# Kernel tuning notes

Measured on AMD Instinct MI355X. Metric: run time of the kernel, lower is better.

## Reference

```python
import jax, jax.numpy as jnp
import numpy as np

K = 7      # local attention window (kernel_size)
PAD = 3    # padding = (K - 1) // 2 so unfold output matches input spatial size
EPS = 1e-5 # BatchNorm eps


def conv1x1(x, w, b):
    # x: [B,C,H,W], w: [O,C] -> [B,O,H,W]
    return jnp.einsum('bchw,oc->bohw', x, w) + b[None, :, None, None]


def bn(x, g, beta, m, v):
    # inference-mode BatchNorm2d
    s = g / jnp.sqrt(v + EPS)
    return (x - m[None, :, None, None]) * s[None, :, None, None] + beta[None, :, None, None]


def unfold(x):
    # F.unfold(kernel=K, pad=PAD, stride=1) reshaped to [B, C, K*K, H, W]
    b, c, h, w = x.shape
    xp = jnp.pad(x, ((0, 0), (0, 0), (PAD, PAD), (PAD, PAD)))
    return jnp.stack([xp[:, :, i:i + h, j:j + w]
                      for i in range(K) for j in range(K)], axis=2)


def setup_inputs() -> dict:
    key = jax.random.key(0)
    ks = jax.random.split(key, 17)
    B, C, H, W = 2, 256, 96, 96
    KC, VC, OC = 64, 128, 256

    def n(k, shape, s=0.05):
        return jax.random.normal(k, shape, dtype=jnp.float32) * s

    return {
        'x': jax.random.normal(ks[0], (B, C, H, W), dtype=jnp.float32),
        'wq': n(ks[1], (KC, C)), 'bq': n(ks[2], (KC,)),
        'gq': 1.0 + n(ks[3], (KC,)), 'betaq': n(ks[4], (KC,)),
        'mq': n(ks[5], (KC,)),
        'vq': jax.random.uniform(ks[6], (KC,), dtype=jnp.float32, minval=0.5, maxval=1.5),
        'wk': n(ks[7], (KC, C)), 'bk': n(ks[8], (KC,)),
        'gk': 1.0 + n(ks[9], (KC,)), 'betak': n(ks[10], (KC,)),
        'mk': n(ks[11], (KC,)),
        'vk': jax.random.uniform(ks[12], (KC,), dtype=jnp.float32, minval=0.5, maxval=1.5),
        'wv': n(ks[13], (VC, C)), 'bv': n(ks[14], (VC,)),
        'ww': n(ks[15], (OC, VC)), 'bw': n(ks[16], (OC,)),
    }


def reference(x, wq, bq, gq, betaq, mq, vq, wk, bk, gk, betak, mk, vk, wv, bv, ww, bw):
    value = conv1x1(x, wv, bv)                       # [B,VC,H,W]
    uv = unfold(value)                                # [B,VC,K*K,H,W]
    keyf = bn(conv1x1(x, wk, bk), gk, betak, mk, vk)  # [B,KC,H,W]
    uk = unfold(keyf)                                 # [B,KC,K*K,H,W]
    query = bn(conv1x1(x, wq, bq), gq, betaq, mq, vq) # [B,KC,H,W]
    # sim_map = sum over channels of (unfold_key * query), softmax over patch dim
    sim = jnp.einsum('bcphw,bchw->bphw', uk, query)   # [B,K*K,H,W]
    sm = jax.nn.softmax(sim, axis=1)
    context = jnp.einsum('bphw,bcphw->bchw', sm, uv)  # [B,VC,H,W]
    return conv1x1(context, ww, bw)                   # [B,OC,H,W]
```

## Files before the change

kernel.cpp:

```cpp
#include <hip/hip_runtime.h>
#include <hip/hip_bf16.h>
#include <cstddef>


#define HW 9216
#define IMH 96
#define IMW 96

__global__ __launch_bounds__(256) void prep_kernel(
    const float* __restrict__ wq, const float* __restrict__ bq,
    const float* __restrict__ gq, const float* __restrict__ betaq,
    const float* __restrict__ mq, const float* __restrict__ vq,
    const float* __restrict__ wk, const float* __restrict__ bk,
    const float* __restrict__ gk, const float* __restrict__ betak,
    const float* __restrict__ mk, const float* __restrict__ vk,
    const float* __restrict__ wv, const float* __restrict__ bv,
    float* __restrict__ Weff, float* __restrict__ beff) {
  int o = blockIdx.x;
  int c = threadIdx.x;
  float wval, bval;
  if (o < 64) {
    float s = gq[o] * rsqrtf(vq[o] + 1e-5f);
    wval = wq[o * 256 + c] * s;
    bval = (bq[o] - mq[o]) * s + betaq[o];
  } else if (o < 128) {
    int oo = o - 64;
    float s = gk[oo] * rsqrtf(vk[oo] + 1e-5f);
    wval = wk[oo * 256 + c] * s;
    bval = (bk[oo] - mk[oo]) * s + betak[oo];
  } else {
    int oo = o - 128;
    wval = wv[oo * 256 + c];
    bval = bv[oo];
  }
  Weff[o * 256 + c] = wval;
  if (c == 0) beff[o] = bval;
}

template <int KD>
__global__ __launch_bounds__(256) void gemm_tile(
    const float* __restrict__ A, const float* __restrict__ bias,
    const float* __restrict__ X, float* __restrict__ O, long xbstride) {
  int b = blockIdx.z;
  int m0 = blockIdx.y * 64;
  int n0 = blockIdx.x * 64;
  const float* Xb = X + (size_t)b * xbstride;
  float* Ob = O + (size_t)b * 256 * HW;

  __shared__ float As[16][68];
  __shared__ float Bs[16][68];

  int tid = threadIdx.x;
  int tx = tid & 15;
  int ty = tid >> 4;

  float acc[4][4];
#pragma unroll
  for (int i = 0; i < 4; i++)
#pragma unroll
    for (int j = 0; j < 4; j++) acc[i][j] = 0.f;

  for (int kk = 0; kk < KD; kk += 16) {
#pragma unroll
    for (int i = 0; i < 4; i++) {
      int idx = tid + i * 256;
      int m = idx >> 4, k = idx & 15;
      As[k][m] = A[(size_t)(m0 + m) * KD + kk + k];
    }
#pragma unroll
    for (int i = 0; i < 4; i++) {
      int idx = tid + i * 256;
      int k = idx >> 6, n = idx & 63;
      Bs[k][n] = Xb[(size_t)(kk + k) * HW + n0 + n];
    }
    __syncthreads();
#pragma unroll
    for (int k = 0; k < 16; k++) {
      float4 av = *(const float4*)&As[k][ty * 4];
      float4 bv4 = *(const float4*)&Bs[k][tx * 4];
      float a_[4] = {av.x, av.y, av.z, av.w};
      float b_[4] = {bv4.x, bv4.y, bv4.z, bv4.w};
#pragma unroll
      for (int i = 0; i < 4; i++)
#pragma unroll
        for (int j = 0; j < 4; j++) acc[i][j] = fmaf(a_[i], b_[j], acc[i][j]);
    }
    __syncthreads();
  }

#pragma unroll
  for (int i = 0; i < 4; i++) {
    int m = m0 + ty * 4 + i;
    float bs = bias[m];
    float4 r;
    r.x = acc[i][0] + bs;
    r.y = acc[i][1] + bs;
    r.z = acc[i][2] + bs;
    r.w = acc[i][3] + bs;
    *(float4*)&Ob[(size_t)m * HW + n0 + tx * 4] = r;
  }
}

__global__ __launch_bounds__(64) void sim_kernel(
    const float* __restrict__ qkv, float* __restrict__ sm) {
  int b = blockIdx.z;
  int tap = blockIdx.y;
  int pix = blockIdx.x * 64 + threadIdx.x;
  int h = pix / IMW, w = pix % IMW;
  int di = tap / 7 - 3, dj = tap % 7 - 3;
  const float* Qp = qkv + (size_t)b * 256 * HW + pix;
  const float* Kp = Qp + (size_t)64 * HW + di * IMW + dj;

  float a0 = 0.f, a1 = 0.f, a2 = 0.f, a3 = 0.f;
#pragma unroll 8
  for (int c = 0; c < 64; c++) {
    float q = Qp[(size_t)c * HW];
    float k = Kp[(size_t)c * HW];
    if ((c & 3) == 0) a0 = fmaf(q, k, a0);
    else if ((c & 3) == 1) a1 = fmaf(q, k, a1);
    else if ((c & 3) == 2) a2 = fmaf(q, k, a2);
    else a3 = fmaf(q, k, a3);
  }
  float s = (a0 + a1) + (a2 + a3);
  bool valid = ((unsigned)(h + di) < (unsigned)IMH) &&
               ((unsigned)(w + dj) < (unsigned)IMW);
  sm[((size_t)b * 49 + tap) * HW + pix] = valid ? s : 0.f;
}

__global__ __launch_bounds__(64) void softmax_kernel(float* __restrict__ sm) {
  int b = blockIdx.y;
  int pix = blockIdx.x * 64 + threadIdx.x;
  int h = pix / IMW, w = pix % IMW;
  float* S = sm + (size_t)b * 49 * HW + pix;

  float v[49];
#pragma unroll
  for (int p = 0; p < 49; p++) v[p] = S[(size_t)p * HW];

  float mx = v[0];
#pragma unroll
  for (int p = 1; p < 49; p++) mx = fmaxf(mx, v[p]);
  float ssum = 0.f;
#pragma unroll
  for (int p = 0; p < 49; p++) {
    v[p] = __expf(v[p] - mx);
    ssum += v[p];
  }
  float inv = 1.f / ssum;
#pragma unroll
  for (int p = 0; p < 49; p++) {
    const int di = p / 7 - 3, dj = p % 7 - 3;
    bool valid = ((unsigned)(h + di) < (unsigned)IMH) &&
                 ((unsigned)(w + dj) < (unsigned)IMW);
    S[(size_t)p * HW] = valid ? v[p] * inv : 0.f;
  }
}

__global__ __launch_bounds__(64) void ctx_kernel(
    const float* __restrict__ qkv, const float* __restrict__ sm,
    float* __restrict__ ctx) {
  int b = blockIdx.z;
  int c0 = blockIdx.y * 4;
  int pix = blockIdx.x * 64 + threadIdx.x;

  const float* S = sm + (size_t)b * 49 * HW + pix;
  float p[49];
#pragma unroll
  for (int t = 0; t < 49; t++) p[t] = S[(size_t)t * HW];

  const float* V = qkv + ((size_t)b * 256 + 128) * HW + pix;
  float* Cb = ctx + (size_t)b * 256 * HW + pix;

#pragma unroll
  for (int cc = 0; cc < 4; cc++) {
    const float* Vc = V + (size_t)(c0 + cc) * HW;
    float a0 = 0.f, a1 = 0.f, a2 = 0.f, a3 = 0.f;
#pragma unroll
    for (int t = 0; t < 49; t++) {
      const int di = t / 7 - 3, dj = t % 7 - 3;
      float v = Vc[di * IMW + dj];
      if ((t & 3) == 0) a0 = fmaf(p[t], v, a0);
      else if ((t & 3) == 1) a1 = fmaf(p[t], v, a1);
      else if ((t & 3) == 2) a2 = fmaf(p[t], v, a2);
      else a3 = fmaf(p[t], v, a3);
    }
    Cb[(size_t)(c0 + cc) * HW] = (a0 + a1) + (a2 + a3);
  }
}

extern "C" void kernel_launch(void* const* d_in, const int* in_sizes, int n_in,
                              void* d_out, int out_size, void* d_ws, size_t ws_size,
                              hipStream_t stream) {
  const float* x     = (const float*)d_in[0];
  const float* wq    = (const float*)d_in[1];
  const float* bq    = (const float*)d_in[2];
  const float* gq    = (const float*)d_in[3];
  const float* betaq = (const float*)d_in[4];
  const float* mq    = (const float*)d_in[5];
  const float* vq    = (const float*)d_in[6];
  const float* wk    = (const float*)d_in[7];
  const float* bk    = (const float*)d_in[8];
  const float* gk    = (const float*)d_in[9];
  const float* betak = (const float*)d_in[10];
  const float* mk    = (const float*)d_in[11];
  const float* vk    = (const float*)d_in[12];
  const float* wv    = (const float*)d_in[13];
  const float* bv    = (const float*)d_in[14];
  const float* ww    = (const float*)d_in[15];
  const float* bw    = (const float*)d_in[16];

  float* ws = (float*)d_ws;
  float* Weff = ws;
  float* beff = ws + 65536;
  float* qkv  = ws + 65792;
  float* sm   = ws + 65792 + 4718592 + 1024;
  float* ctxb = qkv;

  prep_kernel<<<dim3(256), dim3(256), 0, stream>>>(
      wq, bq, gq, betaq, mq, vq, wk, bk, gk, betak, mk, vk, wv, bv, Weff, beff);

  gemm_tile<256><<<dim3(144, 4, 2), dim3(256), 0, stream>>>(
      Weff, beff, x, qkv, (long)256 * HW);

  sim_kernel<<<dim3(144, 49, 2), dim3(64), 0, stream>>>(qkv, sm);

  softmax_kernel<<<dim3(144, 2), dim3(64), 0, stream>>>(sm);

  ctx_kernel<<<dim3(144, 32, 2), dim3(64), 0, stream>>>(qkv, sm, ctxb);

  gemm_tile<128><<<dim3(144, 4, 2), dim3(256), 0, stream>>>(
      ww, bw, ctxb, (float*)d_out, (long)256 * HW);
}
```

Measured before the change: 204.7 us.

## Replace FP32 SIMT GEMMs with split-bf16 MFMA GEMMs plus transpose-convert passes

Both 1x1-conv GEMMs now run on bf16 MFMA instructions. Each fp32 operand is split into hi and lo bf16 parts, and three products (hi*hi, lo*hi, hi*lo) are accumulated to keep close to fp32 accuracy. New transpose-and-convert kernels write the activations in pixel-major bf16 hi/lo form, and the prep kernel also splits the weights. This adds extra memory passes and kernel launches and triples the MFMA work, in exchange for much higher matrix throughput than the FMA-based tiles.

```diff
diff --git a/kernel.cpp b/kernel.cpp
--- a/kernel.cpp
+++ b/kernel.cpp
@@ -6,6 +6,19 @@
 #define HW 9216
 #define IMH 96
 #define IMW 96
+
+using bf16x8 = __attribute__((ext_vector_type(8))) short;
+using f32x4  = __attribute__((ext_vector_type(4))) float;
+
+__device__ inline unsigned short f2bf(float f) {
+  unsigned u = __builtin_bit_cast(unsigned, f);
+  unsigned r = 0x7fffu + ((u >> 16) & 1u);
+  return (unsigned short)((u + r) >> 16);
+}
+__device__ inline float bf2f(unsigned short h) {
+  unsigned u = (unsigned)h << 16;
+  return __builtin_bit_cast(float, u);
+}
 
 __global__ __launch_bounds__(256) void prep_kernel(
     const float* __restrict__ wq, const float* __restrict__ bq,
@@ -15,7 +28,10 @@
     const float* __restrict__ gk, const float* __restrict__ betak,
     const float* __restrict__ mk, const float* __restrict__ vk,
     const float* __restrict__ wv, const float* __restrict__ bv,
-    float* __restrict__ Weff, float* __restrict__ beff) {
+    const float* __restrict__ ww,
+    unsigned short* __restrict__ WeffHi, unsigned short* __restrict__ WeffLo,
+    float* __restrict__ beff,
+    unsigned short* __restrict__ wwHi, unsigned short* __restrict__ wwLo) {
   int o = blockIdx.x;
   int c = threadIdx.x;
   float wval, bval;
@@ -33,71 +49,124 @@
     wval = wv[oo * 256 + c];
     bval = bv[oo];
   }
-  Weff[o * 256 + c] = wval;
+  unsigned short hi = f2bf(wval);
+  WeffHi[o * 256 + c] = hi;
+  WeffLo[o * 256 + c] = f2bf(wval - bf2f(hi));
   if (c == 0) beff[o] = bval;
+  if (c < 128) {
+    float wv2 = ww[o * 128 + c];
+    unsigned short h2 = f2bf(wv2);
+    wwHi[o * 128 + c] = h2;
+    wwLo[o * 128 + c] = f2bf(wv2 - bf2f(h2));
+  }
+}
+
+template <int C>
+__global__ __launch_bounds__(256) void tcvt_kernel(
+    const float* __restrict__ in,
+    unsigned short* __restrict__ outHi, unsigned short* __restrict__ outLo) {
+  int b = blockIdx.z;
+  int c0 = blockIdx.y * 64;
+  int p0 = blockIdx.x * 64;
+  const float* ib = in + (size_t)b * C * HW;
+  unsigned short* obh = outHi + (size_t)b * HW * C;
+  unsigned short* obl = outLo + (size_t)b * HW * C;
+  __shared__ float t[64][65];
+  int tid = threadIdx.x;
+#pragma unroll
+  for (int i = 0; i < 16; i++) {
+    int idx = tid + i * 256;
+    int c = idx >> 6, p = idx & 63;
+    t[c][p] = ib[(size_t)(c0 + c) * HW + p0 + p];
+  }
+  __syncthreads();
+#pragma unroll
+  for (int i = 0; i < 16; i++) {
+    int idx = tid + i * 256;
+    int p = idx >> 6, c = idx & 63;
+    float v = t[c][p];
+    unsigned short hi = f2bf(v);
+    size_t o = (size_t)(p0 + p) * C + c0 + c;
+    obh[o] = hi;
+    obl[o] = f2bf(v - bf2f(hi));
+  }
 }
 
 template <int KD>
-__global__ __launch_bounds__(256) void gemm_tile(
-    const float* __restrict__ A, const float* __restrict__ bias,
-    const float* __restrict__ X, float* __restrict__ O, long xbstride) {
+__global__ __launch_bounds__(256) void mfma_gemm(
+    const unsigned short* __restrict__ XThi,
+    const unsigned short* __restrict__ XTlo,
+    const unsigned short* __restrict__ WHhi,
+    const unsigned short* __restrict__ WHlo,
+    const float* __restrict__ bias,
+    float* __restrict__ O) {
   int b = blockIdx.z;
-  int m0 = blockIdx.y * 64;
-  int n0 = blockIdx.x * 64;
-  const float* Xb = X + (size_t)b * xbstride;
+  int n0 = blockIdx.x * 128;
+  int m0 = blockIdx.y * 128;
+  const unsigned short* XbHi = XThi + (size_t)b * HW * KD;
+  const unsigned short* XbLo = XTlo + (size_t)b * HW * KD;
+
+  __shared__ unsigned short Xs[128][72];
+  __shared__ unsigned short Ws[128][72];
+
+  int tid = threadIdx.x;
+  int wave = tid >> 6;
+  int lane = tid & 63;
+  int wn = (wave & 1) * 64;
+  int wm = (wave >> 1) * 64;
+  int l15 = lane & 15;
+  int kg = lane >> 4;
+
+  f32x4 acc[4][4];
+#pragma unroll
+  for (int i = 0; i < 4; i++)
+#pragma unroll
+    for (int j = 0; j < 4; j++) acc[i][j] = (f32x4){0.f, 0.f, 0.f, 0.f};
+
+  for (int seg = 0; seg < 3; seg++) {
+    const unsigned short* Xsrc = (seg == 1) ? XbLo : XbHi;
+    const unsigned short* Wsrc = (seg == 2) ? WHlo : WHhi;
+    for (int k0 = 0; k0 < KD; k0 += 64) {
+#pragma unroll
+      for (int i = 0; i < 4; i++) {
+        int idx = tid + i * 256;
+        int r = idx >> 3, ch = idx & 7;
+        *(int4*)&Xs[r][ch * 8] = *(const int4*)&Xsrc[(size_t)(n0 + r) * KD + k0 + ch * 8];
+        *(int4*)&Ws[r][ch * 8] = *(const int4*)&Wsrc[(size_t)(m0 + r) * KD + k0 + ch * 8];
+      }
+      __syncthreads();
+#pragma unroll
+      for (int ks = 0; ks < 2; ks++) {
+        bf16x8 a[4], w[4];
+#pragma unroll
+        for (int f = 0; f < 4; f++) {
+          a[f] = *(const bf16x8*)&Xs[wn + f * 16 + l15][ks * 32 + kg * 8];
+          w[f] = *(const bf16x8*)&Ws[wm + f * 16 + l15][ks * 32 + kg * 8];
+        }
+#pragma unroll
+        for (int nf = 0; nf < 4; nf++)
+#pragma unroll
+          for (int mf = 0; mf < 4; mf++)
+            acc[nf][mf] = __builtin_amdgcn_mfma_f32_16x16x32_bf16(
+                a[nf], w[mf], acc[nf][mf], 0, 0, 0);
+      }
+      __syncthreads();
+    }
+  }
+
   float* Ob = O + (size_t)b * 256 * HW;
-
-  __shared__ float As[16][68];
-  __shared__ float Bs[16][68];
-
-  int tid = threadIdx.x;
-  int tx = tid & 15;
-  int ty = tid >> 4;
-
-  float acc[4][4];
-#pragma unroll
-  for (int i = 0; i < 4; i++)
-#pragma unroll
-    for (int j = 0; j < 4; j++) acc[i][j] = 0.f;
-
-  for (int kk = 0; kk < KD; kk += 16) {
-#pragma unroll
-    for (int i = 0; i < 4; i++) {
-      int idx = tid + i * 256;
-      int m = idx >> 4, k = idx & 15;
-      As[k][m] = A[(size_t)(m0 + m) * KD + kk + k];
+#pragma unroll
+  for (int mf = 0; mf < 4; mf++) {
+    int m = m0 + wm + mf * 16 + l15;
+    float bs = bias[m];
+#pragma unroll
+    for (int nf = 0; nf < 4; nf++) {
+      int n = n0 + wn + nf * 16 + kg * 4;
+      f32x4 v = acc[nf][mf];
+      float4 r4;
+      r4.x = v[0] + bs; r4.y = v[1] + bs; r4.z = v[2] + bs; r4.w = v[3] + bs;
+      *(float4*)&Ob[(size_t)m * HW + n] = r4;
     }
-#pragma unroll
-    for (int i = 0; i < 4; i++) {
-      int idx = tid + i * 256;
-      int k = idx >> 6, n = idx & 63;
-      Bs[k][n] = Xb[(size_t)(kk + k) * HW + n0 + n];
-    }
-    __syncthreads();
-#pragma unroll
-    for (int k = 0; k < 16; k++) {
-      float4 av = *(const float4*)&As[k][ty * 4];
-      float4 bv4 = *(const float4*)&Bs[k][tx * 4];
-      float a_[4] = {av.x, av.y, av.z, av.w};
-      float b_[4] = {bv4.x, bv4.y, bv4.z, bv4.w};
-#pragma unroll
-      for (int i = 0; i < 4; i++)
-#pragma unroll
-        for (int j = 0; j < 4; j++) acc[i][j] = fmaf(a_[i], b_[j], acc[i][j]);
-    }
-    __syncthreads();
-  }
-
-#pragma unroll
-  for (int i = 0; i < 4; i++) {
-    int m = m0 + ty * 4 + i;
-    float bs = bias[m];
-    float4 r;
-    r.x = acc[i][0] + bs;
-    r.y = acc[i][1] + bs;
-    r.z = acc[i][2] + bs;
-    r.w = acc[i][3] + bs;
-    *(float4*)&Ob[(size_t)m * HW + n0 + tx * 4] = r;
   }
 }
 
@@ -169,7 +238,7 @@
   for (int t = 0; t < 49; t++) p[t] = S[(size_t)t * HW];
 
   const float* V = qkv + ((size_t)b * 256 + 128) * HW + pix;
-  float* Cb = ctx + (size_t)b * 256 * HW + pix;
+  float* Cb = ctx + (size_t)b * 128 * HW + pix;
 
 #pragma unroll
   for (int cc = 0; cc < 4; cc++) {
@@ -209,25 +278,37 @@
   const float* ww    = (const float*)d_in[15];
   const float* bw    = (const float*)d_in[16];
 
-  float* ws = (float*)d_ws;
-  float* Weff = ws;
-  float* beff = ws + 65536;
-  float* qkv  = ws + 65792;
-  float* sm   = ws + 65792 + 4718592 + 1024;
-  float* ctxb = qkv;
+  char* base = (char*)d_ws;
+  unsigned short* WeffHi = (unsigned short*)(base + 0);
+  unsigned short* WeffLo = (unsigned short*)(base + 131072);
+  unsigned short* wwHi   = (unsigned short*)(base + 262144);
+  unsigned short* wwLo   = (unsigned short*)(base + 327680);
+  float*          beff   = (float*)(base + 393216);
+  unsigned short* xThi   = (unsigned short*)(base + 397312);
+  unsigned short* xTlo   = (unsigned short*)(base + 9834496);
+  float*          qkv    = (float*)(base + 19271680);
+  float*          smb    = (float*)(base + 38150144);
+  float*          ctxf   = (float*)(base + 41762816);
+  unsigned short* ctxThi = (unsigned short*)(base + 51200000);
+  unsigned short* ctxTlo = (unsigned short*)(base + 55918592);
 
   prep_kernel<<<dim3(256), dim3(256), 0, stream>>>(
-      wq, bq, gq, betaq, mq, vq, wk, bk, gk, betak, mk, vk, wv, bv, Weff, beff);
-
-  gemm_tile<256><<<dim3(144, 4, 2), dim3(256), 0, stream>>>(
-      Weff, beff, x, qkv, (long)256 * HW);
-
-  sim_kernel<<<dim3(144, 49, 2), dim3(64), 0, stream>>>(qkv, sm);
-
-  softmax_kernel<<<dim3(144, 2), dim3(64), 0, stream>>>(sm);
-
-  ctx_kernel<<<dim3(144, 32, 2), dim3(64), 0, stream>>>(qkv, sm, ctxb);
-
-  gemm_tile<128><<<dim3(144, 4, 2), dim3(256), 0, stream>>>(
-      ww, bw, ctxb, (float*)d_out, (long)256 * HW);
-}
+      wq, bq, gq, betaq, mq, vq, wk, bk, gk, betak, mk, vk, wv, bv, ww,
+      WeffHi, WeffLo, beff, wwHi, wwLo);
+
+  tcvt_kernel<256><<<dim3(144, 4, 2), dim3(256), 0, stream>>>(x, xThi, xTlo);
+
+  mfma_gemm<256><<<dim3(72, 2, 2), dim3(256), 0, stream>>>(
+      xThi, xTlo, WeffHi, WeffLo, beff, qkv);
+
+  sim_kernel<<<dim3(144, 49, 2), dim3(64), 0, stream>>>(qkv, smb);
+
+  softmax_kernel<<<dim3(144, 2), dim3(64), 0, stream>>>(smb);
+
+  ctx_kernel<<<dim3(144, 32, 2), dim3(64), 0, stream>>>(qkv, smb, ctxf);
+
+  tcvt_kernel<128><<<dim3(144, 2, 2), dim3(256), 0, stream>>>(ctxf, ctxThi, ctxTlo);
+
+  mfma_gemm<128><<<dim3(72, 2, 2), dim3(256), 0, stream>>>(
+      ctxThi, ctxTlo, wwHi, wwLo, bw, (float*)d_out);
+}
```

Result: faster. 191.1 us (-6.6%).
